# Optimization experiments

Measured on AMD Instinct MI355X. Metric: run time of the kernel, lower is better.

Reference implementation:

```python
import jax, jax.numpy as jnp
import numpy as np

DEPTH = 4
H1 = 64
H2 = 16
NF = 5
L = 10.0
K = 4
DIM = 3
N = 2048
NK = N // 4
FEAT = 1 + 2 * NF * DIM  # r scalar + Nf (cos,sin) pairs of dim components


def _tn(k, shape, std=0.01):
    return jax.random.truncated_normal(k, -2.0, 2.0, shape, jnp.float32) * std


def setup_inputs() -> dict:
    key = jax.random.key(0)
    ks = jax.random.split(key, 16)
    comb0 = 3 * DIM + 3 * FEAT   # combine width at depth 0
    combd = 3 * H1 + 3 * H2      # combine width at later depths
    return {
        "sx": jax.random.uniform(ks[0], (N, DIM), jnp.float32) * L,
        "kpoints": jax.random.normal(ks[1], (2 * NK, DIM), jnp.float32),
        "we0": _tn(ks[2], (comb0, H1)), "be0": jnp.zeros((H1,), jnp.float32),
        "we_rest": _tn(ks[3], (DEPTH - 1, combd, H1)), "be_rest": jnp.zeros((DEPTH - 1, H1), jnp.float32),
        "wee0": _tn(ks[4], (FEAT, H2)), "bee0": jnp.zeros((H2,), jnp.float32),
        "wee_rest": _tn(ks[5], (DEPTH - 2, H2, H2)), "bee_rest": jnp.zeros((DEPTH - 2, H2), jnp.float32),
        "wep0": _tn(ks[6], (FEAT, H2)), "bep0": jnp.zeros((H2,), jnp.float32),
        "wep_rest": _tn(ks[7], (DEPTH - 2, H2, H2)), "bep_rest": jnp.zeros((DEPTH - 2, H2), jnp.float32),
        "orb_w_re": _tn(ks[8], (H1, H1)), "orb_w_im": _tn(ks[9], (H1, H1)),
        "orb_b_re": jnp.zeros((H1,), jnp.float32), "orb_b_im": jnp.zeros((H1,), jnp.float32),
        "w_det": _tn(ks[10], (K, H1, H1)),
        "bf_w": _tn(ks[11], (H1, DIM)),
        "mlp_w1": _tn(ks[12], (DIM, H1)), "mlp_b1": jnp.zeros((H1,), jnp.float32),
        "mlp_w2": _tn(ks[13], (H1, K * (NK - 1))), "mlp_b2": jnp.zeros((K * (NK - 1),), jnp.float32),
    }


def _fourier(rij, r):
    # interleaved [r, cos1, sin1, ..., cosNf, sinNf] like the original
    feats = [r[..., None]]
    for k in range(1, NF + 1):
        ang = (2.0 * np.pi * k / L) * rij
        feats.append(jnp.cos(ang))
        feats.append(jnp.sin(ang))
    return jnp.concatenate(feats, axis=-1)


def _combine(e, ee, ep):
    mm = e.shape[0]
    h = mm // 2
    g1a = jnp.broadcast_to(jnp.mean(e[:h], 0, keepdims=True), e.shape)
    g1b = jnp.broadcast_to(jnp.mean(e[h:], 0, keepdims=True), e.shape)
    g2a = jnp.mean(ee[:h], axis=0)
    g2b = jnp.mean(ee[h:], axis=0)
    g3 = jnp.mean(ep, axis=1)
    return jnp.concatenate([e, g1a, g1b, g2a, g2b, g3], axis=1)


def _forward(sx, kpoints, we0, be0, we_rest, be_rest, wee0, bee0, wee_rest, bee_rest,
             wep0, bep0, wep_rest, bep_rest, orb_w_re, orb_w_im, orb_b_re, orb_b_im,
             w_det, bf_w, mlp_w1, mlp_b1, mlp_w2, mlp_b2):
    n, dim = sx.shape
    m, m2 = n // 2, n // 4
    s, x = sx[:m], sx[m:]
    e = jnp.broadcast_to(kpoints[0][None, :], (m, dim))
    # electron-electron pairwise features (m,m,FEAT)
    rij = x[:, None, :] - x[None, :, :]
    eye = jnp.eye(m, dtype=x.dtype)
    r = jnp.linalg.norm(jnp.sin(np.pi * rij / L) + eye[..., None], axis=-1) * (1.0 - eye) * (L / np.pi)
    ee = _fourier(rij, r)
    # electron-proton pairwise features (m,m,FEAT)
    rij = x[:, None, :] - s[None, :, :]
    r = jnp.linalg.norm(jnp.sin(np.pi * rij / L), axis=-1) * (L / np.pi)
    ep = _fourier(rij, r)
    for d in range(DEPTH - 1):
        f = _combine(e, ee, ep)
        We, be = (we0, be0) if d == 0 else (we_rest[d - 1], be_rest[d - 1])
        Wee, bee = (wee0, bee0) if d == 0 else (wee_rest[d - 1], bee_rest[d - 1])
        Wep, bep = (wep0, bep0) if d == 0 else (wep_rest[d - 1], bep_rest[d - 1])
        e_u = jnp.tanh(f @ We + be)
        ee_u = jnp.tanh(ee @ Wee + bee)
        ep_u = jnp.tanh(ep @ Wep + bep)
        e, ee, ep = (e_u + e, ee_u + ee, ep_u + ep) if d > 0 else (e_u, ee_u, ep_u)
    f = _combine(e, ee, ep)
    e = jnp.tanh(f @ we_rest[-1] + be_rest[-1]) + e
    # complex orbitals and geminal pairing matrix phi: (K, m2, m2)
    orb = e.astype(jnp.complex64) @ (orb_w_re + 1j * orb_w_im) + (orb_b_re + 1j * orb_b_im)
    phi = jnp.einsum('ia,kab,jb->kij', orb[:m2], w_det.astype(jnp.complex64), orb[m2:]) + 1.0
    # backflow coordinates and plane-wave determinant factors
    z = e @ bf_w + x
    nk = kpoints.shape[0] // 2
    norm = 1.0 / L ** (dim / 2)
    D_up = norm * jnp.exp(1j * jnp.einsum('kd,id->ki', kpoints[:nk], z[:m2]))  # (nk, m2)
    D_dn = norm * jnp.exp(1j * jnp.einsum('kd,id->ki', kpoints[nk:], z[m2:]))  # (nk, m2)
    h = jnp.tanh(kpoints[0] @ mlp_w1 + mlp_b1)
    fdet = jax.nn.softplus(h @ mlp_w2 + mlp_b2).reshape(K, nk - 1)
    fdet = jnp.concatenate([jnp.ones((K, 1), fdet.dtype), fdet], axis=1)  # (K, nk)
    D = jnp.einsum('ai,ka,aj->kij', D_up, fdet.astype(D_up.dtype), jnp.conj(D_dn))
    # logdet_matmul: stable log of signed sum of K determinants
    phase, logabs = jnp.linalg.slogdet(D * phi)
    maxl = jnp.max(logabs)
    det = jnp.sum(phase * jnp.exp(logabs - maxl))
    return jnp.log(jnp.abs(det)) + maxl + jnp.log(det / jnp.abs(det))


def reference(sx, kpoints, we0, be0, we_rest, be_rest, wee0, bee0, wee_rest, bee_rest,
              wep0, bep0, wep_rest, bep_rest, orb_w_re, orb_w_im, orb_b_re, orb_b_im,
              w_det, bf_w, mlp_w1, mlp_b1, mlp_w2, mlp_b2):
    return _forward(sx, kpoints, we0, be0, we_rest, be_rest, wee0, bee0, wee_rest, bee_rest,
                    wep0, bep0, wep_rest, bep_rest, orb_w_re, orb_w_im, orb_b_re, orb_b_im,
                    w_det, bf_w, mlp_w1, mlp_b1, mlp_w2, mlp_b2)
```

## Files before the change

### kernel.cpp

```cpp
#include <hip/hip_runtime.h>

typedef unsigned int uint;
typedef unsigned short ushort;

#define M1 1024
#define MH 512
#define PI_F 3.14159265358979323846f
#define LBOX 10.0f
#define NB 32

__device__ __forceinline__ float bf2f(ushort h){ return __uint_as_float(((uint)h)<<16); }
__device__ __forceinline__ ushort f2bf(float f){ uint u = __float_as_uint(f); uint r = (u + 0x7fffu + ((u>>16)&1u))>>16; return (ushort)r; }
__device__ __forceinline__ float ftanh(float x){ float e = __expf(2.f*x); return 1.f - 2.f/(e+1.f); }
__device__ __forceinline__ float2 cmul(float2 a, float2 b){ return make_float2(a.x*b.x - a.y*b.y, a.x*b.y + a.y*b.x); }
__device__ __forceinline__ void cfma(float2& c, float2 a, float2 b){
  c.x = fmaf(a.x,b.x,fmaf(-a.y,b.y,c.x));
  c.y = fmaf(a.x,b.y,fmaf(a.y,b.x,c.y));
}

__device__ __forceinline__ void fourier31(float d0, float d1, float d2, bool diag, float f[31]){
  const float k1 = PI_F / LBOX;
  float s[3], c[3];
  __sincosf(k1*d0, &s[0], &c[0]);
  __sincosf(k1*d1, &s[1], &c[1]);
  __sincosf(k1*d2, &s[2], &c[2]);
  float r = diag ? 0.f : (LBOX/PI_F)*sqrtf(s[0]*s[0]+s[1]*s[1]+s[2]*s[2]);
  f[0] = r;
  float cb[3], sb[3], cc[3], sc[3];
  #pragma unroll
  for (int d=0; d<3; ++d){ cb[d] = 1.f - 2.f*s[d]*s[d]; sb[d] = 2.f*s[d]*c[d]; cc[d]=cb[d]; sc[d]=sb[d]; }
  #pragma unroll
  for (int k=0;k<5;++k){
    #pragma unroll
    for (int d=0; d<3; ++d){ f[1+6*k+d] = cc[d]; f[4+6*k+d] = sc[d]; }
    if (k<4){
      #pragma unroll
      for (int d=0; d<3; ++d){
        float nc = cc[d]*cb[d]-sc[d]*sb[d];
        float ns = sc[d]*cb[d]+cc[d]*sb[d];
        cc[d]=nc; sc[d]=ns;
      }
    }
// ... 32 lines not shown
    ushort lo = f2bf(ftanh(acc[2*h]));
    ushort hi = f2bf(ftanh(acc[2*h+1]));
    u[h] = (uint)lo | ((uint)hi<<16);
  }
  uint4* dst = (uint4*)(out + ((size_t)i*M1 + j)*16);
  dst[0] = make_uint4(u[0],u[1],u[2],u[3]);
  dst[1] = make_uint4(u[4],u[5],u[6],u[7]);
  __shared__ float buf[256*33];
  #pragma unroll
  for (int c=0;c<31;++c) buf[threadIdx.x*33+c] = f[c];
  __syncthreads();
  #pragma unroll
  for (int s=128; s>0; s>>=1){
    if (threadIdx.x < s){
      #pragma unroll
      for (int c=0;c<31;++c) buf[threadIdx.x*33+c] += buf[(threadIdx.x+s)*33+c];
    }
    __syncthreads();
  }
  if (threadIdx.x < 31){
    float* g = (chunk >= 2) ? g2b : g2a;
    atomicAdd(&g[i*31+threadIdx.x], buf[threadIdx.x]);
  }
}

__global__ __launch_bounds__(256) void k_pair0ep(const float* __restrict__ sx,
    const float* __restrict__ W0, const float* __restrict__ b0,
    const float* __restrict__ W1, const float* __restrict__ b1,
    const float* __restrict__ W2, const float* __restrict__ b2,
    float* __restrict__ g3, float* __restrict__ gep1, float* __restrict__ gep2,
    float* __restrict__ gep3){
  int bx = blockIdx.x;
  int i = bx >> 2;
  int chunk = bx & 3;
  int j = (chunk << 8) + threadIdx.x;
  const float* xs = sx + 3*M1;
  float xi0 = xs[3*i], xi1 = xs[3*i+1], xi2 = xs[3*i+2];
  float y0 = sx[3*j], y1 = sx[3*j+1], y2 = sx[3*j+2];
  float f[31];
  fourier31(xi0-y0, xi1-y1, xi2-y2, false, f);
  float acc[16];
  #pragma unroll
  for (int o=0;o<16;++o) acc[o] = b0[o];
  #pragma unroll
  for (int c=0;c<31;++c){ float fv = f[c];
    #pragma unroll
    for (int o=0;o<16;++o) acc[o] = fmaf(fv, W0[c*16+o], acc[o]);
  }
  float hv[16];
  #pragma unroll
  for (int o=0;o<16;++o) hv[o] = ftanh(acc[o]);
  __shared__ float buf[256*49];
  #pragma unroll
  for (int c=0;c<31;++c) buf[threadIdx.x*49+c] = f[c];
  #pragma unroll
  for (int c=0;c<16;++c) buf[threadIdx.x*49+31+c] = hv[c];
  __syncthreads();
  #pragma unroll
  for (int s=128; s>0; s>>=1){
    if (threadIdx.x < s){
      #pragma unroll
      for (int c=0;c<47;++c) buf[threadIdx.x*49+c] += buf[(threadIdx.x+s)*49+c];
    }
    __syncthreads();
  }
  if (threadIdx.x < 31) atomicAdd(&g3[i*31+threadIdx.x], buf[threadIdx.x]);
  else if (threadIdx.x < 47) atomicAdd(&gep1[i*16 + (threadIdx.x-31)], buf[threadIdx.x]);
  float v1[16];
// ... 246 lines not shown
    __syncthreads();
    #pragma unroll
    for (int aa=0; aa<16; ++aa){
      float2 A0 = As[aa*32+i0], A1 = As[aa*32+i0+1];
      float2 B0 = Bs[aa*32+j0], B1 = Bs[aa*32+j0+16];
      cfma(a00,A0,B0); cfma(a01,A0,B1); cfma(a10,A1,B0); cfma(a11,A1,B1);
    }
    __syncthreads();
  }
  float2* Ts = sm;
  float2* Od = sm + 2080;
  for (int t = threadIdx.x; t < 2048; t += 256){
    int il = t >> 6, bc = t & 63;
    Ts[il*65+bc] = T[((size_t)k*512 + ib + il)*64 + bc];
    int oidx = (512 + jb + il)*64 + bc;
    Od[il*65+bc] = make_float2(ore[oidx], oim[oidx]);
  }
  __syncthreads();
  float2 p00={1,0},p01={1,0},p10={1,0},p11={1,0};
  #pragma unroll 8
  for (int bb=0; bb<64; ++bb){
    float2 T0 = Ts[i0*65+bb], T1 = Ts[(i0+1)*65+bb];
    float2 O0 = Od[j0*65+bb], O1 = Od[(j0+16)*65+bb];
    cfma(p00,T0,O0); cfma(p01,T0,O1); cfma(p10,T1,O0); cfma(p11,T1,O1);
  }
  size_t base = ((size_t)k*512 + ib + i0)*512 + jb;
  Mb[base+j0]        = cmul(a00, p00);
  Mb[base+j0+16]     = cmul(a01, p01);
  Mb[base+512+j0]    = cmul(a10, p10);
  Mb[base+512+j0+16] = cmul(a11, p11);
}

__global__ __launch_bounds__(512)
void k_panel(float2* __restrict__ Mb, float2* __restrict__ LinvG,
             int* __restrict__ rowmap, int* __restrict__ swapc, int col0){
  int k = blockIdx.x;
  float2* Mk = Mb + (size_t)k*512*512;
  int R = 512 - col0;
  int R64 = R < 64 ? R : 64;
  int rl = threadIdx.x;
  bool active = rl < R;
  int wv = rl >> 6;
  __shared__ float2 mir[64*33];
  __shared__ float2 Us[NB*33];
  __shared__ float2 dinv[NB];
  __shared__ float2 Ls[NB*NB];
  __shared__ float2 Yv[NB*NB];
  __shared__ int winslot[NB];
  __shared__ int newposS[64];
  int rm_orig = active ? rowmap[k*512 + col0 + rl] : 0;
  float2 X[NB];
  if (rl >= 64 && active){
    const float4* rp = (const float4*)(Mk + (size_t)rm_orig*512 + col0);
    #pragma unroll
    for (int q=0;q<NB/2;++q){ float4 v = rp[q]; X[2*q]=make_float2(v.x,v.y); X[2*q+1]=make_float2(v.z,v.w); }
  }
  if (wv == 0){
    if (rl < R64){
      const float4* rp = (const float4*)(Mk + (size_t)rm_orig*512 + col0);
      #pragma unroll
      for (int q=0;q<NB/2;++q){
        float4 v = rp[q];
        mir[rl*33+2*q]   = make_float2(v.x,v.y);
        mir[rl*33+2*q+1] = make_float2(v.z,v.w);
      }
    }
    bool done = false;
    int winpos = 0;
    for (int cc=0; cc<NB; ++cc){
      bool cand = (rl < R64) && !done;
      float2 cv = make_float2(0.f,0.f);
      if (cand) cv = mir[rl*33+cc];
      float val = cand ? fmaf(cv.x,cv.x,cv.y*cv.y) : -1.f;
      int idx = rl;
      #pragma unroll
      for (int off=32; off>0; off>>=1){
        float ov = __shfl_xor(val, off);
        int   oi = __shfl_xor(idx, off);
        if (ov > val || (ov == val && oi < idx)){ val = ov; idx = oi; }
      }
      int p = idx;
      if (rl == 0) winslot[cc] = p;
      if (rl == p){ done = true; winpos = cc; }
      float2 dg = mir[p*33+cc];
      float dn = 1.f/fmaf(dg.x,dg.x,dg.y*dg.y);
      float2 inv = make_float2(dg.x*dn, -dg.y*dn);
      if (cand && rl != p){
        float2 l = cmul(cv, inv);
        mir[rl*33+cc] = l;
        for (int j=cc+1; j<NB; ++j){
          float2 pr = mir[p*33+j];
          float2 xv = mir[rl*33+j];
          xv.x = fmaf(-l.x, pr.x, fmaf( l.y, pr.y, xv.x));
          xv.y = fmaf(-l.x, pr.y, fmaf(-l.y, pr.x, xv.y));
          mir[rl*33+j] = xv;
        }
      }
    }
    unsigned long long nwmask = __ballot(rl < R64 && !done);
    int np = 0;
    if (rl < R64){
      np = done ? winpos : (NB + (int)__popcll(nwmask & ((1ull<<rl)-1ull)));
      newposS[rl] = np;
      rowmap[k*512 + col0 + np] = rm_orig;
      float4* wp = (float4*)(Mk + (size_t)rm_orig*512 + col0);
      #pragma unroll
      for (int q=0;q<NB/2;++q){
        float2 a = mir[rl*33+2*q], bq = mir[rl*33+2*q+1];
        wp[q] = make_float4(a.x,a.y,bq.x,bq.y);
      }
    }
    {
      int cnt = 0;
      for (int t=0;t<R64;++t){
        int nt = newposS[t];
        if (rl < R64 && t > rl && nt < np) cnt++;
      }
      #pragma unroll
      for (int off=32; off>0; off>>=1) cnt += __shfl_xor(cnt, off);
      if (rl == 0) swapc[k] += cnt;
    }
    if (rl < NB){
      int ws = winslot[rl];
      #pragma unroll
      for (int j=0;j<NB;++j){
        float2 v = mir[ws*33+j];
        Us[rl*33+j] = v;
        float2 lv;
        if      (j <  rl) lv = v;
        else if (j == rl) lv = make_float2(1.f,0.f);
        else              lv = make_float2(0.f,0.f);
        Ls[rl*NB+j] = lv;
      }
      float2 d = Us[rl*33+rl];
      float dn = 1.f/fmaf(d.x,d.x,d.y*d.y);
      dinv[rl] = make_float2(d.x*dn, -d.y*dn);
    }
  }
  __syncthreads();
  if (rl >= 64 && active){
    #pragma unroll
    for (int j=0;j<NB;++j){
      float2 t = X[j];
      #pragma unroll
      for (int q=0;q<NB;++q){
        if (q < j){
          float2 u = Us[q*33+j];
          t.x = fmaf(-X[q].x, u.x, fmaf( X[q].y, u.y, t.x));
          t.y = fmaf(-X[q].x, u.y, fmaf(-X[q].y, u.x, t.y));
        }
      }
      X[j] = cmul(t, dinv[j]);
    }
    float4* wp = (float4*)(Mk + (size_t)rm_orig*512 + col0);
    #pragma unroll
    for (int q=0;q<NB/2;++q) wp[q] = make_float4(X[2*q].x,X[2*q].y,X[2*q+1].x,X[2*q+1].y);
  }
  if (rl < NB){
    for (int i=0;i<NB;++i){
      float2 acc = (i==rl)? make_float2(1.f,0.f) : make_float2(0.f,0.f);
      for (int q=rl; q<i; ++q){
        float2 lv = Ls[i*NB+q];
        float2 yv = Yv[q*NB+rl];
        acc.x = fmaf(-lv.x, yv.x, fmaf( lv.y, yv.y, acc.x));
        acc.y = fmaf(-lv.x, yv.y, fmaf(-lv.y, yv.x, acc.y));
      }
      Yv[i*NB+rl] = acc;
    }
  }
  __syncthreads();
  {
    float4* dst = (float4*)(LinvG + (size_t)k*(NB*NB));
    const float4* src = (const float4*)Yv;
    for (int q=rl; q<NB*NB/2; q+=blockDim.x) dst[q] = src[q];
  }
}

__global__ __launch_bounds__(256) void k_gemm(float2* __restrict__ Mb, const float2* __restrict__ LinvG,
                                              const int* __restrict__ rowmap, int col0){
  int k = blockIdx.z;
  float2* Mk = Mb + (size_t)k*512*512;
  int e0 = col0 + NB;
  int r0 = e0 + blockIdx.x*32;
  int j0c = e0 + blockIdx.y*32;
  int tid = threadIdx.x;
  int jl = tid & 31, rg = tid >> 5;
  __shared__ float2 As[NB*33];
  __shared__ float2 Bs[NB*33];
  __shared__ float2 Av[NB*33];
  __shared__ float2 Li[NB*NB];
  __shared__ int prA[32];
  __shared__ int prB[NB];
  if (tid < 32) prA[tid] = rowmap[k*512 + r0 + tid];
  else if (tid < 64) prB[tid-32] = rowmap[k*512 + col0 + (tid-32)];
  {
    const float4* src = (const float4*)(LinvG + (size_t)k*(NB*NB));
    float4* dst = (float4*)Li;
    for (int q=tid; q<NB*NB/2; q+=256) dst[q] = src[q];
  }
  __syncthreads();
  #pragma unroll
  for (int s=0;s<4;++s){
    int a = rg + 8*s;
    Av[a*33 + jl] = Mk[(size_t)prB[a]*512 + j0c + jl];
  }
  for (int t=tid; t<1024; t+=256){
    int rl = t >> 5, kk = t & 31;
    As[kk*33+rl] = Mk[(size_t)prA[rl]*512 + col0 + kk];
  }
  __syncthreads();
  #pragma unroll
  for (int s=0;s<4;++s){
    int m = rg + 8*s;
    float2 acc = make_float2(0.f,0.f);
    #pragma unroll 8
    for (int a=0;a<NB;++a) cfma(acc, Li[m*NB+a], Av[a*33+jl]);
    Bs[m*33+jl] = acc;
  }
  __syncthreads();
  int i0 = (tid >> 4)*2, j0 = (tid & 15)*2;
  float2 a00={0,0},a01={0,0},a10={0,0},a11={0,0};
  #pragma unroll 16
  for (int kk=0;kk<NB;++kk){
    float2 A0 = As[kk*33+i0], A1 = As[kk*33+i0+1];
    float2 B0 = Bs[kk*33+j0], B1 = Bs[kk*33+j0+1];
    cfma(a00,A0,B0); cfma(a01,A0,B1); cfma(a10,A1,B0); cfma(a11,A1,B1);
  }
  size_t ro0 = (size_t)prA[i0]*512 + j0c + j0;
  size_t ro1 = (size_t)prA[i0+1]*512 + j0c + j0;
  float2 c0 = Mk[ro0];   c0.x-=a00.x; c0.y-=a00.y; Mk[ro0]=c0;
  float2 c1 = Mk[ro0+1]; c1.x-=a01.x; c1.y-=a01.y; Mk[ro0+1]=c1;
  float2 c2 = Mk[ro1];   c2.x-=a10.x; c2.y-=a10.y; Mk[ro1]=c2;
  float2 c3 = Mk[ro1+1]; c3.x-=a11.x; c3.y-=a11.y; Mk[ro1+1]=c3;
}

__global__ void k_det(const float2* __restrict__ Mb, const int* __restrict__ rowmap,
                      const int* __restrict__ swapc, float* __restrict__ out, int out_size){
  int tid = threadIdx.x;
  int k = tid >> 6, lane = tid & 63;
  const float2* Mk = Mb + (size_t)k*512*512;
  double la = 0.0, ang = 0.0;
  for (int q=0;q<8;++q){
    int i = lane*8 + q;
    int pr = rowmap[k*512 + i];
    float2 u = Mk[(size_t)pr*512+i];
    double re = (double)u.x, im = (double)u.y;
    la += 0.5*log(re*re + im*im);
    ang += atan2(im, re);
  }
  #pragma unroll
  for (int off=32; off>0; off>>=1){
    la += __shfl_down(la, off);
    ang += __shfl_down(ang, off);
  }
  __shared__ double las[4], angs[4];
  if (lane==0){
    las[k] = la;
    angs[k] = ang + 3.14159265358979323846*(double)(swapc[k] & 1);
  }
  __syncthreads();
  if (tid==0){
    double mx = las[0];
    for (int q=1;q<4;++q) mx = fmax(mx, las[q]);
    double sre=0.0, sim=0.0;
    for (int q=0;q<4;++q){
      double w = exp(las[q]-mx);
      sre += w*cos(angs[q]);
      sim += w*sin(angs[q]);
    }
    double mag = sqrt(sre*sre+sim*sim);
    out[0] = (float)(log(mag)+mx);
    if (out_size > 1) out[1] = (float)atan2(sim, sre);
    for (int q=2;q<out_size;++q) out[q] = 0.f;
  }
}

extern "C" void kernel_launch(void* const* d_in, const int* in_sizes, int n_in,
                              void* d_out, int out_size, void* d_ws, size_t ws_size,
                              hipStream_t stream){
  const float* sx   = (const float*)d_in[0];
  const float* kp   = (const float*)d_in[1];
  const float* we0  = (const float*)d_in[2];
  const float* be0  = (const float*)d_in[3];
  const float* weR  = (const float*)d_in[4];
  const float* beR  = (const float*)d_in[5];
  const float* wee0 = (const float*)d_in[6];
  const float* bee0 = (const float*)d_in[7];
  const float* weeR = (const float*)d_in[8];
  const float* beeR = (const float*)d_in[9];
  const float* wep0 = (const float*)d_in[10];
  const float* bep0 = (const float*)d_in[11];
  const float* wepR = (const float*)d_in[12];
  const float* bepR = (const float*)d_in[13];
  const float* owre = (const float*)d_in[14];
  const float* owim = (const float*)d_in[15];
  const float* obre = (const float*)d_in[16];
  const float* obim = (const float*)d_in[17];
  const float* wdet = (const float*)d_in[18];
  const float* bfw  = (const float*)d_in[19];
  const float* mw1  = (const float*)d_in[20];
  const float* mb1  = (const float*)d_in[21];
  const float* mw2  = (const float*)d_in[22];
  const float* mb2  = (const float*)d_in[23];

  char* ws = (char*)d_ws;
  size_t off = 0;
  auto alloc = [&](size_t bytes)->char*{
    char* p = ws + off;
    off = (off + bytes + 255) & ~(size_t)255;
    return p;
  };
  ushort* ee   = (ushort*)alloc(33554432);
  float2* Mb   = (float2*)alloc(8388608);
  float2* U    = (float2*)alloc(2097152);
  float2* V    = (float2*)alloc(2097152);
  float2* T    = (float2*)alloc(1048576);
  float*  eS   = (float*)alloc(1048576);
  float*  ore  = (float*)alloc(262144);
  float*  oim  = (float*)alloc(262144);
  float*  z    = (float*)alloc(12288);
  float*  fdet = (float*)alloc(8192);
  float2* Linv = (float2*)alloc(131072);
  int*    rowmap = (int*)alloc(8192);
  char*   zst  = ws + off;
  float*  g2a0 = (float*)alloc(126976);
  float*  g2b0 = (float*)alloc(126976);
  float*  g30  = (float*)alloc(126976);
  float*  geeA = (float*)alloc(196608);
  float*  geeB = (float*)alloc(196608);
  float*  gep  = (float*)alloc(196608);
  float*  g1s  = (float*)alloc(1536);
  int*    swpc = (int*)alloc(16);
  int zn = (int)(((char*)(swpc+4) - zst)/4);

  float* e1 = eS;           float* e2 = eS + 65536;
  float* e3 = eS + 131072;  float* e4 = eS + 196608;
  float* geeA1 = geeA;      float* geeA2 = geeA+16384; float* geeA3 = geeA+32768;
  float* geeB1 = geeB;      float* geeB2 = geeB+16384; float* geeB3 = geeB+32768;
  float* gep1  = gep;       float* gep2  = gep+16384;  float* gep3  = gep+32768;
  float* g1s1 = g1s; float* g1s2 = g1s+128; float* g1s3 = g1s+256;

  k_init<<<256,256,0,stream>>>((float*)zst, zn, rowmap);
  k_pair0ee<<<4096,256,0,stream>>>(sx, wee0, bee0, ee, g2a0, g2b0);
  k_pair0ep<<<4096,256,0,stream>>>(sx, wep0, bep0, wepR, bepR, wepR+256, bepR+16,
                                   g30, gep1, gep2, gep3);
  k_e0<<<256,256,0,stream>>>(kp, g2a0, g2b0, g30, we0, be0, e1, g1s1);
  k_gee<<<128,256,0,stream>>>(ee, geeA1, geeB1);
  k_eupd<<<256,256,0,stream>>>(e1, e2, weR, beR, g1s1, geeA1, geeB1, gep1, g1s2);
  k_pairU<<<4096,256,0,stream>>>(ee, weeR, beeR);
  k_gee<<<128,256,0,stream>>>(ee, geeA2, geeB2);
  k_eupd<<<256,256,0,stream>>>(e2, e3, weR+240*64, beR+64, g1s2, geeA2, geeB2, gep2, g1s3);
  k_pairU<<<4096,256,0,stream>>>(ee, weeR+256, beeR+16);
  k_gee<<<128,256,0,stream>>>(ee, geeA3, geeB3);
  k_eupd<<<256,256,0,stream>>>(e3, e4, weR+2*240*64, beR+128, g1s3, geeA3, geeB3, gep3, nullptr);
  k_orbz<<<256,256,0,stream>>>(e4, owre, owim, obre, obim, bfw, sx, ore, oim, z);
  k_uvTf<<<2568,256,0,stream>>>(kp, z, ore, oim, wdet, mw1, mb1, mw2, mb2, U, V, T, fdet);
  k_M<<<1024,256,0,stream>>>(U, V, fdet, T, ore, oim, Mb);
  for (int tpan=0;tpan<16;++tpan){
    int col0 = tpan*NB;
    int R = 512 - col0;
    int Rpad = (R + 63) & ~63;
    k_panel<<<4, Rpad, 0, stream>>>(Mb, Linv, rowmap, swpc, col0);
    if (tpan < 15){
      int nch = 15 - tpan;
      k_gemm<<<dim3(nch,nch,4),256,0,stream>>>(Mb, Linv, rowmap, col0);
    }
  }
  k_det<<<1,256,0,stream>>>(Mb, rowmap, swpc, (float*)d_out, out_size);
  (void)in_sizes; (void)n_in; (void)ws_size;
}
```

Baseline: 1.844 ms.

## Fuse blocked LU panel, trailing update and det into one persistent kernel

Replaces the 31 alternating panel/GEMM launches and the final determinant launch with a single persistent kernel of 256 blocks. The blocks step through the panels and separate the phases with an atomic-counter grid barrier. Trailing-update tiles are distributed across blocks in a strided job loop. This removes per-launch overhead on the sequential LU chain, but it relies on all 256 blocks being co-resident and adds spin-barrier cost. Panel steps also use only 4 of the 256 blocks while the rest wait.

```diff
diff --git a/kernel.cpp b/kernel.cpp
--- a/kernel.cpp
+++ b/kernel.cpp
@@ -420,246 +420,273 @@
 }
 
 __global__ __launch_bounds__(512)
-void k_panel(float2* __restrict__ Mb, float2* __restrict__ LinvG,
-             int* __restrict__ rowmap, int* __restrict__ swapc, int col0){
-  int k = blockIdx.x;
-  float2* Mk = Mb + (size_t)k*512*512;
-  int R = 512 - col0;
-  int R64 = R < 64 ? R : 64;
-  int rl = threadIdx.x;
-  bool active = rl < R;
-  int wv = rl >> 6;
-  __shared__ float2 mir[64*33];
-  __shared__ float2 Us[NB*33];
+void k_lu(float2* __restrict__ Mb, float2* __restrict__ LinvG,
+          int* __restrict__ rowmap, int* __restrict__ swapc,
+          int* __restrict__ bar, float* __restrict__ out, int out_size){
+  int bid = blockIdx.x;
+  int tid = threadIdx.x;
+  __shared__ float2 smA[64*33];
+  __shared__ float2 smB[32*33];
+  __shared__ float2 smC[32*32];
+  __shared__ float2 smD[32*32];
   __shared__ float2 dinv[NB];
-  __shared__ float2 Ls[NB*NB];
-  __shared__ float2 Yv[NB*NB];
   __shared__ int winslot[NB];
   __shared__ int newposS[64];
-  int rm_orig = active ? rowmap[k*512 + col0 + rl] : 0;
-  float2 X[NB];
-  if (rl >= 64 && active){
-    const float4* rp = (const float4*)(Mk + (size_t)rm_orig*512 + col0);
-    #pragma unroll
-    for (int q=0;q<NB/2;++q){ float4 v = rp[q]; X[2*q]=make_float2(v.x,v.y); X[2*q+1]=make_float2(v.z,v.w); }
-  }
-  if (wv == 0){
-    if (rl < R64){
-      const float4* rp = (const float4*)(Mk + (size_t)rm_orig*512 + col0);
-      #pragma unroll
-      for (int q=0;q<NB/2;++q){
-        float4 v = rp[q];
-        mir[rl*33+2*q]   = make_float2(v.x,v.y);
-        mir[rl*33+2*q+1] = make_float2(v.z,v.w);
-      }
-    }
-    bool done = false;
-    int winpos = 0;
-    for (int cc=0; cc<NB; ++cc){
-      bool cand = (rl < R64) && !done;
-      float2 cv = make_float2(0.f,0.f);
-      if (cand) cv = mir[rl*33+cc];
-      float val = cand ? fmaf(cv.x,cv.x,cv.y*cv.y) : -1.f;
-      int idx = rl;
+  __shared__ int prA[32];
+  __shared__ int prB[32];
+  __shared__ double las[4], angs[4];
+  int ph = 0;
+  const int G = (int)gridDim.x;
+
+  for (int t=0; t<16; ++t){
+    int col0 = t*NB;
+    if (bid < 4){
+      int k = bid;
+      float2* Mk = Mb + (size_t)k*512*512;
+      int R = 512 - col0;
+      int R64 = R < 64 ? R : 64;
+      int rl = tid;
+      bool active = rl < R;
+      int wv = rl >> 6;
+      float2* mir = smA;
+      float2* Us  = smB;
+      float2* Ls  = smC;
+      float2* Yv  = smD;
+      int rm_orig = active ? rowmap[k*512 + col0 + rl] : 0;
+      float2 X[NB];
+      if (rl >= 64 && active){
+        const float4* rp = (const float4*)(Mk + (size_t)rm_orig*512 + col0);
+        #pragma unroll
+        for (int q=0;q<NB/2;++q){ float4 v = rp[q]; X[2*q]=make_float2(v.x,v.y); X[2*q+1]=make_float2(v.z,v.w); }
+      }
+      if (wv == 0){
+        if (rl < R64){
+          const float4* rp = (const float4*)(Mk + (size_t)rm_orig*512 + col0);
+          #pragma unroll
+          for (int q=0;q<NB/2;++q){
+            float4 v = rp[q];
+            mir[rl*33+2*q]   = make_float2(v.x,v.y);
+            mir[rl*33+2*q+1] = make_float2(v.z,v.w);
+          }
+        }
+        bool done = false;
+        int winpos = 0;
+        for (int cc=0; cc<NB; ++cc){
+          bool cand = (rl < R64) && !done;
+          float2 cv = make_float2(0.f,0.f);
+          if (cand) cv = mir[rl*33+cc];
+          float val = cand ? fmaf(cv.x,cv.x,cv.y*cv.y) : -1.f;
+          int idx = rl;
+          #pragma unroll
+          for (int off=32; off>0; off>>=1){
+            float ov = __shfl_xor(val, off);
+            int   oi = __shfl_xor(idx, off);
+            if (ov > val || (ov == val && oi < idx)){ val = ov; idx = oi; }
+          }
+          int p = idx;
+          if (rl == 0) winslot[cc] = p;
+          if (rl == p){ done = true; winpos = cc; }
+          float2 dg = mir[p*33+cc];
+          float dn = 1.f/fmaf(dg.x,dg.x,dg.y*dg.y);
+          float2 inv = make_float2(dg.x*dn, -dg.y*dn);
+          if (cand && rl != p){
+            float2 l = cmul(cv, inv);
+            mir[rl*33+cc] = l;
+            for (int j=cc+1; j<NB; ++j){
+              float2 pr = mir[p*33+j];
+              float2 xv = mir[rl*33+j];
+              xv.x = fmaf(-l.x, pr.x, fmaf( l.y, pr.y, xv.x));
+              xv.y = fmaf(-l.x, pr.y, fmaf(-l.y, pr.x, xv.y));
+              mir[rl*33+j] = xv;
+            }
+          }
+        }
+        unsigned long long nwmask = __ballot(rl < R64 && !done);
+        int np = 0;
+        if (rl < R64){
+          np = done ? winpos : (NB + (int)__popcll(nwmask & ((1ull<<rl)-1ull)));
+          newposS[rl] = np;
+          rowmap[k*512 + col0 + np] = rm_orig;
+          float4* wp = (float4*)(Mk + (size_t)rm_orig*512 + col0);
+          #pragma unroll
+          for (int q=0;q<NB/2;++q){
+            float2 a = mir[rl*33+2*q], bq = mir[rl*33+2*q+1];
+            wp[q] = make_float4(a.x,a.y,bq.x,bq.y);
+          }
+        }
+        {
+          int cnt = 0;
+          for (int tt=0;tt<R64;++tt){
+            int nt = newposS[tt];
+            if (rl < R64 && tt > rl && nt < np) cnt++;
+          }
+          #pragma unroll
+          for (int off=32; off>0; off>>=1) cnt += __shfl_xor(cnt, off);
+          if (rl == 0) swapc[k] += cnt;
+        }
+        if (rl < NB){
+          int ws = winslot[rl];
+          #pragma unroll
+          for (int j=0;j<NB;++j){
+            float2 v = mir[ws*33+j];
+            Us[rl*33+j] = v;
+            float2 lv;
+            if      (j <  rl) lv = v;
+            else if (j == rl) lv = make_float2(1.f,0.f);
+            else              lv = make_float2(0.f,0.f);
+            Ls[rl*NB+j] = lv;
+          }
+          float2 d = Us[rl*33+rl];
+          float dn = 1.f/fmaf(d.x,d.x,d.y*d.y);
+          dinv[rl] = make_float2(d.x*dn, -d.y*dn);
+        }
+      }
+      __syncthreads();
+      if (rl >= 64 && active){
+        #pragma unroll
+        for (int j=0;j<NB;++j){
+          float2 tt = X[j];
+          #pragma unroll
+          for (int q=0;q<NB;++q){
+            if (q < j){
+              float2 u = Us[q*33+j];
+              tt.x = fmaf(-X[q].x, u.x, fmaf( X[q].y, u.y, tt.x));
+              tt.y = fmaf(-X[q].x, u.y, fmaf(-X[q].y, u.x, tt.y));
+            }
+          }
+          X[j] = cmul(tt, dinv[j]);
+        }
+        float4* wp = (float4*)(Mk + (size_t)rm_orig*512 + col0);
+        #pragma unroll
+        for (int q=0;q<NB/2;++q) wp[q] = make_float4(X[2*q].x,X[2*q].y,X[2*q+1].x,X[2*q+1].y);
+      }
+      if (rl < NB){
+        for (int i=0;i<NB;++i){
+          float2 acc = (i==rl)? make_float2(1.f,0.f) : make_float2(0.f,0.f);
+          for (int q=rl; q<i; ++q){
+            float2 lv = Ls[i*NB+q];
+            float2 yv = Yv[q*NB+rl];
+            acc.x = fmaf(-lv.x, yv.x, fmaf( lv.y, yv.y, acc.x));
+            acc.y = fmaf(-lv.x, yv.y, fmaf(-lv.y, yv.x, acc.y));
+          }
+          Yv[i*NB+rl] = acc;
+        }
+      }
+      __syncthreads();
+      ((float4*)(LinvG + (size_t)k*(NB*NB)))[rl] = ((const float4*)Yv)[rl];
+    }
+    ph++;
+    __threadfence();
+    __syncthreads();
+    if (tid == 0){
+      atomicAdd(bar, 1);
+      while (__hip_atomic_load(bar, __ATOMIC_RELAXED, __HIP_MEMORY_SCOPE_AGENT) < ph*G)
+        __builtin_amdgcn_s_sleep(2);
+    }
+    __syncthreads();
+    __threadfence();
+    if (t < 15){
+      int nch = 15 - t;
+      int e0 = col0 + NB;
+      int jobs = 4*nch*nch;
+      float2* Av = smA;
+      float2* Bs = smA + 1056;
+      float2* As = smB;
+      float2* Li = smC;
+      int jl = tid & 31;
+      int rg = tid >> 5;
+      for (int job = bid; job < jobs; job += G){
+        int kq = job / (nch*nch);
+        int rem = job - kq*nch*nch;
+        int bx = rem / nch, by = rem - bx*nch;
+        float2* Mk = Mb + (size_t)kq*512*512;
+        int r0 = e0 + bx*32;
+        int j0c = e0 + by*32;
+        if (tid < 32) prA[tid] = rowmap[kq*512 + r0 + tid];
+        else if (tid < 64) prB[tid-32] = rowmap[kq*512 + col0 + (tid-32)];
+        ((float4*)Li)[tid] = ((const float4*)(LinvG + (size_t)kq*(NB*NB)))[tid];
+        __syncthreads();
+        Av[rg*33+jl]      = Mk[(size_t)prB[rg]*512 + j0c + jl];
+        Av[(rg+16)*33+jl] = Mk[(size_t)prB[rg+16]*512 + j0c + jl];
+        #pragma unroll
+        for (int s2=0;s2<2;++s2){
+          int t2 = tid + 512*s2;
+          int rl2 = t2 >> 5, kk2 = t2 & 31;
+          As[kk2*33 + rl2] = Mk[(size_t)prA[rl2]*512 + col0 + kk2];
+        }
+        __syncthreads();
+        #pragma unroll
+        for (int s2=0;s2<2;++s2){
+          int m = rg + 16*s2;
+          float2 acc = make_float2(0.f,0.f);
+          #pragma unroll 8
+          for (int a=0;a<NB;++a) cfma(acc, Li[m*NB+a], Av[a*33+jl]);
+          Bs[m*33+jl] = acc;
+        }
+        __syncthreads();
+        float2 acc0 = make_float2(0.f,0.f), acc1 = make_float2(0.f,0.f);
+        #pragma unroll 16
+        for (int kk=0;kk<NB;++kk){
+          float2 B0 = Bs[kk*33+jl];
+          cfma(acc0, As[kk*33+rg], B0);
+          cfma(acc1, As[kk*33+rg+16], B0);
+        }
+        size_t ro0 = (size_t)prA[rg]*512 + j0c + jl;
+        size_t ro1 = (size_t)prA[rg+16]*512 + j0c + jl;
+        float2 c0 = Mk[ro0]; c0.x-=acc0.x; c0.y-=acc0.y; Mk[ro0]=c0;
+        float2 c1 = Mk[ro1]; c1.x-=acc1.x; c1.y-=acc1.y; Mk[ro1]=c1;
+        __syncthreads();
+      }
+      ph++;
+      __threadfence();
+      __syncthreads();
+      if (tid == 0){
+        atomicAdd(bar, 1);
+        while (__hip_atomic_load(bar, __ATOMIC_RELAXED, __HIP_MEMORY_SCOPE_AGENT) < ph*G)
+          __builtin_amdgcn_s_sleep(2);
+      }
+      __syncthreads();
+      __threadfence();
+    }
+  }
+  if (bid == 0){
+    double la = 0.0, ang = 0.0;
+    if (tid < 256){
+      int kq = tid >> 6, lane = tid & 63;
+      const float2* Mk = Mb + (size_t)kq*512*512;
+      for (int q=0;q<8;++q){
+        int i = lane*8 + q;
+        int pr = rowmap[kq*512 + i];
+        float2 u = Mk[(size_t)pr*512+i];
+        double re = (double)u.x, im = (double)u.y;
+        la += 0.5*log(re*re + im*im);
+        ang += atan2(im, re);
+      }
       #pragma unroll
       for (int off=32; off>0; off>>=1){
-        float ov = __shfl_xor(val, off);
-        int   oi = __shfl_xor(idx, off);
-        if (ov > val || (ov == val && oi < idx)){ val = ov; idx = oi; }
-      }
-      int p = idx;
-      if (rl == 0) winslot[cc] = p;
-      if (rl == p){ done = true; winpos = cc; }
-      float2 dg = mir[p*33+cc];
-      float dn = 1.f/fmaf(dg.x,dg.x,dg.y*dg.y);
-      float2 inv = make_float2(dg.x*dn, -dg.y*dn);
-      if (cand && rl != p){
-        float2 l = cmul(cv, inv);
-        mir[rl*33+cc] = l;
-        for (int j=cc+1; j<NB; ++j){
-          float2 pr = mir[p*33+j];
-          float2 xv = mir[rl*33+j];
-          xv.x = fmaf(-l.x, pr.x, fmaf( l.y, pr.y, xv.x));
-          xv.y = fmaf(-l.x, pr.y, fmaf(-l.y, pr.x, xv.y));
-          mir[rl*33+j] = xv;
-        }
-      }
-    }
-    unsigned long long nwmask = __ballot(rl < R64 && !done);
-    int np = 0;
-    if (rl < R64){
-      np = done ? winpos : (NB + (int)__popcll(nwmask & ((1ull<<rl)-1ull)));
-      newposS[rl] = np;
-      rowmap[k*512 + col0 + np] = rm_orig;
-      float4* wp = (float4*)(Mk + (size_t)rm_orig*512 + col0);
-      #pragma unroll
-      for (int q=0;q<NB/2;++q){
-        float2 a = mir[rl*33+2*q], bq = mir[rl*33+2*q+1];
-        wp[q] = make_float4(a.x,a.y,bq.x,bq.y);
-      }
-    }
-    {
-      int cnt = 0;
-      for (int t=0;t<R64;++t){
-        int nt = newposS[t];
-        if (rl < R64 && t > rl && nt < np) cnt++;
-      }
-      #pragma unroll
-      for (int off=32; off>0; off>>=1) cnt += __shfl_xor(cnt, off);
-      if (rl == 0) swapc[k] += cnt;
-    }
-    if (rl < NB){
-      int ws = winslot[rl];
-      #pragma unroll
-      for (int j=0;j<NB;++j){
-        float2 v = mir[ws*33+j];
-        Us[rl*33+j] = v;
-        float2 lv;
-        if      (j <  rl) lv = v;
-        else if (j == rl) lv = make_float2(1.f,0.f);
-        else              lv = make_float2(0.f,0.f);
-        Ls[rl*NB+j] = lv;
-      }
-      float2 d = Us[rl*33+rl];
-      float dn = 1.f/fmaf(d.x,d.x,d.y*d.y);
-      dinv[rl] = make_float2(d.x*dn, -d.y*dn);
-    }
-  }
-  __syncthreads();
-  if (rl >= 64 && active){
-    #pragma unroll
-    for (int j=0;j<NB;++j){
-      float2 t = X[j];
-      #pragma unroll
-      for (int q=0;q<NB;++q){
-        if (q < j){
-          float2 u = Us[q*33+j];
-          t.x = fmaf(-X[q].x, u.x, fmaf( X[q].y, u.y, t.x));
-          t.y = fmaf(-X[q].x, u.y, fmaf(-X[q].y, u.x, t.y));
-        }
-      }
-      X[j] = cmul(t, dinv[j]);
-    }
-    float4* wp = (float4*)(Mk + (size_t)rm_orig*512 + col0);
-    #pragma unroll
-    for (int q=0;q<NB/2;++q) wp[q] = make_float4(X[2*q].x,X[2*q].y,X[2*q+1].x,X[2*q+1].y);
-  }
-  if (rl < NB){
-    for (int i=0;i<NB;++i){
-      float2 acc = (i==rl)? make_float2(1.f,0.f) : make_float2(0.f,0.f);
-      for (int q=rl; q<i; ++q){
-        float2 lv = Ls[i*NB+q];
-        float2 yv = Yv[q*NB+rl];
-        acc.x = fmaf(-lv.x, yv.x, fmaf( lv.y, yv.y, acc.x));
-        acc.y = fmaf(-lv.x, yv.y, fmaf(-lv.y, yv.x, acc.y));
-      }
-      Yv[i*NB+rl] = acc;
-    }
-  }
-  __syncthreads();
-  {
-    float4* dst = (float4*)(LinvG + (size_t)k*(NB*NB));
-    const float4* src = (const float4*)Yv;
-    for (int q=rl; q<NB*NB/2; q+=blockDim.x) dst[q] = src[q];
-  }
-}
-
-__global__ __launch_bounds__(256) void k_gemm(float2* __restrict__ Mb, const float2* __restrict__ LinvG,
-                                              const int* __restrict__ rowmap, int col0){
-  int k = blockIdx.z;
-  float2* Mk = Mb + (size_t)k*512*512;
-  int e0 = col0 + NB;
-  int r0 = e0 + blockIdx.x*32;
-  int j0c = e0 + blockIdx.y*32;
-  int tid = threadIdx.x;
-  int jl = tid & 31, rg = tid >> 5;
-  __shared__ float2 As[NB*33];
-  __shared__ float2 Bs[NB*33];
-  __shared__ float2 Av[NB*33];
-  __shared__ float2 Li[NB*NB];
-  __shared__ int prA[32];
-  __shared__ int prB[NB];
-  if (tid < 32) prA[tid] = rowmap[k*512 + r0 + tid];
-  else if (tid < 64) prB[tid-32] = rowmap[k*512 + col0 + (tid-32)];
-  {
-    const float4* src = (const float4*)(LinvG + (size_t)k*(NB*NB));
-    float4* dst = (float4*)Li;
-    for (int q=tid; q<NB*NB/2; q+=256) dst[q] = src[q];
-  }
-  __syncthreads();
-  #pragma unroll
-  for (int s=0;s<4;++s){
-    int a = rg + 8*s;
-    Av[a*33 + jl] = Mk[(size_t)prB[a]*512 + j0c + jl];
-  }
-  for (int t=tid; t<1024; t+=256){
-    int rl = t >> 5, kk = t & 31;
-    As[kk*33+rl] = Mk[(size_t)prA[rl]*512 + col0 + kk];
-  }
-  __syncthreads();
-  #pragma unroll
-  for (int s=0;s<4;++s){
-    int m = rg + 8*s;
-    float2 acc = make_float2(0.f,0.f);
-    #pragma unroll 8
-    for (int a=0;a<NB;++a) cfma(acc, Li[m*NB+a], Av[a*33+jl]);
-    Bs[m*33+jl] = acc;
-  }
-  __syncthreads();
-  int i0 = (tid >> 4)*2, j0 = (tid & 15)*2;
-  float2 a00={0,0},a01={0,0},a10={0,0},a11={0,0};
-  #pragma unroll 16
-  for (int kk=0;kk<NB;++kk){
-    float2 A0 = As[kk*33+i0], A1 = As[kk*33+i0+1];
-    float2 B0 = Bs[kk*33+j0], B1 = Bs[kk*33+j0+1];
-    cfma(a00,A0,B0); cfma(a01,A0,B1); cfma(a10,A1,B0); cfma(a11,A1,B1);
-  }
-  size_t ro0 = (size_t)prA[i0]*512 + j0c + j0;
-  size_t ro1 = (size_t)prA[i0+1]*512 + j0c + j0;
-  float2 c0 = Mk[ro0];   c0.x-=a00.x; c0.y-=a00.y; Mk[ro0]=c0;
-  float2 c1 = Mk[ro0+1]; c1.x-=a01.x; c1.y-=a01.y; Mk[ro0+1]=c1;
-  float2 c2 = Mk[ro1];   c2.x-=a10.x; c2.y-=a10.y; Mk[ro1]=c2;
-  float2 c3 = Mk[ro1+1]; c3.x-=a11.x; c3.y-=a11.y; Mk[ro1+1]=c3;
-}
-
-__global__ void k_det(const float2* __restrict__ Mb, const int* __restrict__ rowmap,
-                      const int* __restrict__ swapc, float* __restrict__ out, int out_size){
-  int tid = threadIdx.x;
-  int k = tid >> 6, lane = tid & 63;
-  const float2* Mk = Mb + (size_t)k*512*512;
-  double la = 0.0, ang = 0.0;
-  for (int q=0;q<8;++q){
-    int i = lane*8 + q;
-    int pr = rowmap[k*512 + i];
-    float2 u = Mk[(size_t)pr*512+i];
-    double re = (double)u.x, im = (double)u.y;
-    la += 0.5*log(re*re + im*im);
-    ang += atan2(im, re);
-  }
-  #pragma unroll
-  for (int off=32; off>0; off>>=1){
-    la += __shfl_down(la, off);
-    ang += __shfl_down(ang, off);
-  }
-  __shared__ double las[4], angs[4];
-  if (lane==0){
-    las[k] = la;
-    angs[k] = ang + 3.14159265358979323846*(double)(swapc[k] & 1);
-  }
-  __syncthreads();
-  if (tid==0){
-    double mx = las[0];
-    for (int q=1;q<4;++q) mx = fmax(mx, las[q]);
-    double sre=0.0, sim=0.0;
-    for (int q=0;q<4;++q){
-      double w = exp(las[q]-mx);
-      sre += w*cos(angs[q]);
-      sim += w*sin(angs[q]);
-    }
-    double mag = sqrt(sre*sre+sim*sim);
-    out[0] = (float)(log(mag)+mx);
-    if (out_size > 1) out[1] = (float)atan2(sim, sre);
-    for (int q=2;q<out_size;++q) out[q] = 0.f;
+        la += __shfl_down(la, off);
+        ang += __shfl_down(ang, off);
+      }
+      if (lane==0){
+        las[kq] = la;
+        angs[kq] = ang + 3.14159265358979323846*(double)(swapc[kq] & 1);
+      }
+    }
+    __syncthreads();
+    if (tid==0){
+      double mx = las[0];
+      for (int q=1;q<4;++q) mx = fmax(mx, las[q]);
+      double sre=0.0, sim=0.0;
+      for (int q=0;q<4;++q){
+        double w = exp(las[q]-mx);
+        sre += w*cos(angs[q]);
+        sim += w*sin(angs[q]);
+      }
+      double mag = sqrt(sre*sre+sim*sim);
+      out[0] = (float)(log(mag)+mx);
+      if (out_size > 1) out[1] = (float)atan2(sim, sre);
+      for (int q=2;q<out_size;++q) out[q] = 0.f;
+    }
   }
 }
 
@@ -719,7 +746,8 @@
   float*  gep  = (float*)alloc(196608);
   float*  g1s  = (float*)alloc(1536);
   int*    swpc = (int*)alloc(16);
-  int zn = (int)(((char*)(swpc+4) - zst)/4);
+  int*    bar  = (int*)alloc(256);
+  int zn = (int)(((char*)bar + 256 - zst)/4);
 
   float* e1 = eS;           float* e2 = eS + 65536;
   float* e3 = eS + 131072;  float* e4 = eS + 196608;
@@ -744,16 +772,6 @@
   k_orbz<<<256,256,0,stream>>>(e4, owre, owim, obre, obim, bfw, sx, ore, oim, z);
   k_uvTf<<<2568,256,0,stream>>>(kp, z, ore, oim, wdet, mw1, mb1, mw2, mb2, U, V, T, fdet);
   k_M<<<1024,256,0,stream>>>(U, V, fdet, T, ore, oim, Mb);
-  for (int tpan=0;tpan<16;++tpan){
-    int col0 = tpan*NB;
-    int R = 512 - col0;
-    int Rpad = (R + 63) & ~63;
-    k_panel<<<4, Rpad, 0, stream>>>(Mb, Linv, rowmap, swpc, col0);
-    if (tpan < 15){
-      int nch = 15 - tpan;
-      k_gemm<<<dim3(nch,nch,4),256,0,stream>>>(Mb, Linv, rowmap, col0);
-    }
-  }
-  k_det<<<1,256,0,stream>>>(Mb, rowmap, swpc, (float*)d_out, out_size);
+  k_lu<<<256,512,0,stream>>>(Mb, Linv, rowmap, swpc, bar, (float*)d_out, out_size);
   (void)in_sizes; (void)n_in; (void)ws_size;
 }
```

New measurement: 3.683 ms. 99.8% more time.

## Widen LU panel block from 32 to 64 columns, halving panel/GEMM launches

Applied to the files above, without the earlier changes.

Raises the blocked-LU panel width to 64, so each panel factors 64 rows by pivot search with the whole wave and does the trailing triangular solve in two 32-column halves. Only 8 panel and 7 GEMM rounds are launched instead of 16 and 15, which cuts the serial launch and sync chain of the complex LU factorization. The cost is a longer serial pivot loop per panel, more shared memory and registers in the panel kernel, and a deeper inner dimension in the GEMM. The separate L buffer is dropped and read straight from the mirror array.

```diff
diff --git a/kernel.cpp b/kernel.cpp
--- a/kernel.cpp
+++ b/kernel.cpp
@@ -7,7 +7,7 @@
 #define MH 512
 #define PI_F 3.14159265358979323846f
 #define LBOX 10.0f
-#define NB 32
+#define NB 64
 
 __device__ __forceinline__ float bf2f(ushort h){ return __uint_as_float(((uint)h)<<16); }
 __device__ __forceinline__ ushort f2bf(float f){ uint u = __float_as_uint(f); uint r = (u + 0x7fffu + ((u>>16)&1u))>>16; return (ushort)r; }
@@ -106,8 +106,7 @@
     float* __restrict__ gep3){
   int bx = blockIdx.x;
   int i = bx >> 2;
-  int chunk = bx & 3;
-  int j = (chunk << 8) + threadIdx.x;
+  int j = ((bx & 3) << 8) + threadIdx.x;
   const float* xs = sx + 3*M1;
   float xi0 = xs[3*i], xi1 = xs[3*i+1], xi2 = xs[3*i+2];
   float y0 = sx[3*j], y1 = sx[3*j+1], y2 = sx[3*j+2];
@@ -424,41 +423,29 @@
              int* __restrict__ rowmap, int* __restrict__ swapc, int col0){
   int k = blockIdx.x;
   float2* Mk = Mb + (size_t)k*512*512;
-  int R = 512 - col0;
-  int R64 = R < 64 ? R : 64;
   int rl = threadIdx.x;
-  bool active = rl < R;
   int wv = rl >> 6;
-  __shared__ float2 mir[64*33];
-  __shared__ float2 Us[NB*33];
-  __shared__ float2 dinv[NB];
-  __shared__ float2 Ls[NB*NB];
-  __shared__ float2 Yv[NB*NB];
-  __shared__ int winslot[NB];
+  __shared__ float2 mir[64*65];
+  __shared__ float2 Us[64*65];
+  __shared__ float2 Yv[64*64];
+  __shared__ float2 dinv[64];
+  __shared__ int winslot[64];
   __shared__ int newposS[64];
-  int rm_orig = active ? rowmap[k*512 + col0 + rl] : 0;
-  float2 X[NB];
-  if (rl >= 64 && active){
+  int rm_orig = rowmap[k*512 + col0 + rl];
+  if (wv == 0){
     const float4* rp = (const float4*)(Mk + (size_t)rm_orig*512 + col0);
     #pragma unroll
-    for (int q=0;q<NB/2;++q){ float4 v = rp[q]; X[2*q]=make_float2(v.x,v.y); X[2*q+1]=make_float2(v.z,v.w); }
-  }
-  if (wv == 0){
-    if (rl < R64){
-      const float4* rp = (const float4*)(Mk + (size_t)rm_orig*512 + col0);
-      #pragma unroll
-      for (int q=0;q<NB/2;++q){
-        float4 v = rp[q];
-        mir[rl*33+2*q]   = make_float2(v.x,v.y);
-        mir[rl*33+2*q+1] = make_float2(v.z,v.w);
-      }
+    for (int q=0;q<32;++q){
+      float4 v = rp[q];
+      mir[rl*65+2*q]   = make_float2(v.x,v.y);
+      mir[rl*65+2*q+1] = make_float2(v.z,v.w);
     }
     bool done = false;
     int winpos = 0;
-    for (int cc=0; cc<NB; ++cc){
-      bool cand = (rl < R64) && !done;
+    for (int cc=0; cc<64; ++cc){
+      bool cand = !done;
       float2 cv = make_float2(0.f,0.f);
-      if (cand) cv = mir[rl*33+cc];
+      if (cand) cv = mir[rl*65+cc];
       float val = cand ? fmaf(cv.x,cv.x,cv.y*cv.y) : -1.f;
       int idx = rl;
       #pragma unroll
@@ -470,97 +457,123 @@
       int p = idx;
       if (rl == 0) winslot[cc] = p;
       if (rl == p){ done = true; winpos = cc; }
-      float2 dg = mir[p*33+cc];
+      float2 dg = mir[p*65+cc];
       float dn = 1.f/fmaf(dg.x,dg.x,dg.y*dg.y);
       float2 inv = make_float2(dg.x*dn, -dg.y*dn);
       if (cand && rl != p){
         float2 l = cmul(cv, inv);
-        mir[rl*33+cc] = l;
-        for (int j=cc+1; j<NB; ++j){
-          float2 pr = mir[p*33+j];
-          float2 xv = mir[rl*33+j];
+        mir[rl*65+cc] = l;
+        for (int j=cc+1; j<64; ++j){
+          float2 pr = mir[p*65+j];
+          float2 xv = mir[rl*65+j];
           xv.x = fmaf(-l.x, pr.x, fmaf( l.y, pr.y, xv.x));
           xv.y = fmaf(-l.x, pr.y, fmaf(-l.y, pr.x, xv.y));
-          mir[rl*33+j] = xv;
+          mir[rl*65+j] = xv;
         }
       }
     }
-    unsigned long long nwmask = __ballot(rl < R64 && !done);
-    int np = 0;
-    if (rl < R64){
-      np = done ? winpos : (NB + (int)__popcll(nwmask & ((1ull<<rl)-1ull)));
-      newposS[rl] = np;
-      rowmap[k*512 + col0 + np] = rm_orig;
-      float4* wp = (float4*)(Mk + (size_t)rm_orig*512 + col0);
-      #pragma unroll
-      for (int q=0;q<NB/2;++q){
-        float2 a = mir[rl*33+2*q], bq = mir[rl*33+2*q+1];
-        wp[q] = make_float4(a.x,a.y,bq.x,bq.y);
-      }
+    newposS[rl] = winpos;
+    rowmap[k*512 + col0 + winpos] = rm_orig;
+    float4* wp = (float4*)(Mk + (size_t)rm_orig*512 + col0);
+    #pragma unroll
+    for (int q=0;q<32;++q){
+      float2 a = mir[rl*65+2*q], bq = mir[rl*65+2*q+1];
+      wp[q] = make_float4(a.x,a.y,bq.x,bq.y);
     }
     {
       int cnt = 0;
-      for (int t=0;t<R64;++t){
-        int nt = newposS[t];
-        if (rl < R64 && t > rl && nt < np) cnt++;
-      }
+      for (int t2=rl+1; t2<64; ++t2) if (newposS[t2] < winpos) cnt++;
       #pragma unroll
       for (int off=32; off>0; off>>=1) cnt += __shfl_xor(cnt, off);
       if (rl == 0) swapc[k] += cnt;
     }
-    if (rl < NB){
+    {
       int ws = winslot[rl];
-      #pragma unroll
-      for (int j=0;j<NB;++j){
-        float2 v = mir[ws*33+j];
-        Us[rl*33+j] = v;
-        float2 lv;
-        if      (j <  rl) lv = v;
-        else if (j == rl) lv = make_float2(1.f,0.f);
-        else              lv = make_float2(0.f,0.f);
-        Ls[rl*NB+j] = lv;
-      }
-      float2 d = Us[rl*33+rl];
+      #pragma unroll 8
+      for (int j=0;j<64;++j) Us[rl*65+j] = mir[ws*65+j];
+      float2 d = Us[rl*65+rl];
       float dn = 1.f/fmaf(d.x,d.x,d.y*d.y);
       dinv[rl] = make_float2(d.x*dn, -d.y*dn);
     }
   }
   __syncthreads();
-  if (rl >= 64 && active){
-    #pragma unroll
-    for (int j=0;j<NB;++j){
+  if (rl >= 64){
+    float2 X[32];
+    {
+      const float4* rpA = (const float4*)(Mk + (size_t)rm_orig*512 + col0);
+      #pragma unroll
+      for (int q=0;q<16;++q){ float4 v = rpA[q]; X[2*q]=make_float2(v.x,v.y); X[2*q+1]=make_float2(v.z,v.w); }
+    }
+    #pragma unroll
+    for (int j=0;j<32;++j){
       float2 t = X[j];
       #pragma unroll
-      for (int q=0;q<NB;++q){
+      for (int q=0;q<32;++q){
         if (q < j){
-          float2 u = Us[q*33+j];
+          float2 u = Us[q*65+j];
           t.x = fmaf(-X[q].x, u.x, fmaf( X[q].y, u.y, t.x));
           t.y = fmaf(-X[q].x, u.y, fmaf(-X[q].y, u.x, t.y));
         }
       }
       X[j] = cmul(t, dinv[j]);
     }
-    float4* wp = (float4*)(Mk + (size_t)rm_orig*512 + col0);
-    #pragma unroll
-    for (int q=0;q<NB/2;++q) wp[q] = make_float4(X[2*q].x,X[2*q].y,X[2*q+1].x,X[2*q+1].y);
-  }
-  if (rl < NB){
-    for (int i=0;i<NB;++i){
+    {
+      float4* wpA = (float4*)(Mk + (size_t)rm_orig*512 + col0);
+      #pragma unroll
+      for (int q=0;q<16;++q) wpA[q] = make_float4(X[2*q].x,X[2*q].y,X[2*q+1].x,X[2*q+1].y);
+    }
+    float2 X2[32];
+    {
+      const float4* rpB = (const float4*)(Mk + (size_t)rm_orig*512 + col0 + 32);
+      #pragma unroll
+      for (int q=0;q<16;++q){ float4 v = rpB[q]; X2[2*q]=make_float2(v.x,v.y); X2[2*q+1]=make_float2(v.z,v.w); }
+    }
+    for (int q=0;q<32;++q){
+      float2 x1 = Mk[(size_t)rm_orig*512 + col0 + q];
+      #pragma unroll
+      for (int j=0;j<32;++j){
+        float2 u = Us[q*65+32+j];
+        X2[j].x = fmaf(-x1.x, u.x, fmaf( x1.y, u.y, X2[j].x));
+        X2[j].y = fmaf(-x1.x, u.y, fmaf(-x1.y, u.x, X2[j].y));
+      }
+    }
+    #pragma unroll
+    for (int j=0;j<32;++j){
+      float2 t = X2[j];
+      #pragma unroll
+      for (int q=0;q<32;++q){
+        if (q < j){
+          float2 u = Us[(32+q)*65+32+j];
+          t.x = fmaf(-X2[q].x, u.x, fmaf( X2[q].y, u.y, t.x));
+          t.y = fmaf(-X2[q].x, u.y, fmaf(-X2[q].y, u.x, t.y));
+        }
+      }
+      X2[j] = cmul(t, dinv[32+j]);
+    }
+    {
+      float4* wpB = (float4*)(Mk + (size_t)rm_orig*512 + col0 + 32);
+      #pragma unroll
+      for (int q=0;q<16;++q) wpB[q] = make_float4(X2[2*q].x,X2[2*q].y,X2[2*q+1].x,X2[2*q+1].y);
+    }
+  }
+  if (rl < 64){
+    for (int i=0;i<64;++i){
       float2 acc = (i==rl)? make_float2(1.f,0.f) : make_float2(0.f,0.f);
+      int wsi = winslot[i];
       for (int q=rl; q<i; ++q){
-        float2 lv = Ls[i*NB+q];
-        float2 yv = Yv[q*NB+rl];
+        float2 lv = mir[wsi*65+q];
+        float2 yv = Yv[q*64+rl];
         acc.x = fmaf(-lv.x, yv.x, fmaf( lv.y, yv.y, acc.x));
         acc.y = fmaf(-lv.x, yv.y, fmaf(-lv.y, yv.x, acc.y));
       }
-      Yv[i*NB+rl] = acc;
+      Yv[i*64+rl] = acc;
     }
   }
   __syncthreads();
   {
-    float4* dst = (float4*)(LinvG + (size_t)k*(NB*NB));
+    float4* dst = (float4*)(LinvG + (size_t)k*4096);
     const float4* src = (const float4*)Yv;
-    for (int q=rl; q<NB*NB/2; q+=blockDim.x) dst[q] = src[q];
+    for (int q=rl; q<2048; q+=blockDim.x) dst[q] = src[q];
   }
 }
 
@@ -573,53 +586,53 @@
   int j0c = e0 + blockIdx.y*32;
   int tid = threadIdx.x;
   int jl = tid & 31, rg = tid >> 5;
-  __shared__ float2 As[NB*33];
-  __shared__ float2 Bs[NB*33];
-  __shared__ float2 Av[NB*33];
-  __shared__ float2 Li[NB*NB];
+  __shared__ float2 As[64*33];
+  __shared__ float2 Bs[64*33];
+  __shared__ float2 Av[64*33];
+  __shared__ float2 Li[64*64];
   __shared__ int prA[32];
-  __shared__ int prB[NB];
+  __shared__ int prB[64];
   if (tid < 32) prA[tid] = rowmap[k*512 + r0 + tid];
-  else if (tid < 64) prB[tid-32] = rowmap[k*512 + col0 + (tid-32)];
+  else if (tid < 96) prB[tid-32] = rowmap[k*512 + col0 + (tid-32)];
   {
-    const float4* src = (const float4*)(LinvG + (size_t)k*(NB*NB));
+    const float4* src = (const float4*)(LinvG + (size_t)k*4096);
     float4* dst = (float4*)Li;
-    for (int q=tid; q<NB*NB/2; q+=256) dst[q] = src[q];
-  }
-  __syncthreads();
-  #pragma unroll
-  for (int s=0;s<4;++s){
+    for (int q=tid; q<2048; q+=256) dst[q] = src[q];
+  }
+  __syncthreads();
+  #pragma unroll
+  for (int s=0;s<8;++s){
     int a = rg + 8*s;
     Av[a*33 + jl] = Mk[(size_t)prB[a]*512 + j0c + jl];
   }
-  for (int t=tid; t<1024; t+=256){
-    int rl = t >> 5, kk = t & 31;
-    As[kk*33+rl] = Mk[(size_t)prA[rl]*512 + col0 + kk];
-  }
-  __syncthreads();
-  #pragma unroll
-  for (int s=0;s<4;++s){
+  for (int t=tid; t<2048; t+=256){
+    int rl2 = t >> 6, kk2 = t & 63;
+    As[kk2*33 + rl2] = Mk[(size_t)prA[rl2]*512 + col0 + kk2];
+  }
+  __syncthreads();
+  #pragma unroll
+  for (int s=0;s<8;++s){
     int m = rg + 8*s;
     float2 acc = make_float2(0.f,0.f);
-    #pragma unroll 8
-    for (int a=0;a<NB;++a) cfma(acc, Li[m*NB+a], Av[a*33+jl]);
+    #pragma unroll 16
+    for (int a=0;a<64;++a) cfma(acc, Li[m*64+a], Av[a*33+jl]);
     Bs[m*33+jl] = acc;
   }
   __syncthreads();
-  int i0 = (tid >> 4)*2, j0 = (tid & 15)*2;
+  int i0 = (tid >> 4)*2, j0 = tid & 15;
   float2 a00={0,0},a01={0,0},a10={0,0},a11={0,0};
   #pragma unroll 16
-  for (int kk=0;kk<NB;++kk){
+  for (int kk=0;kk<64;++kk){
     float2 A0 = As[kk*33+i0], A1 = As[kk*33+i0+1];
-    float2 B0 = Bs[kk*33+j0], B1 = Bs[kk*33+j0+1];
+    float2 B0 = Bs[kk*33+j0], B1 = Bs[kk*33+j0+16];
     cfma(a00,A0,B0); cfma(a01,A0,B1); cfma(a10,A1,B0); cfma(a11,A1,B1);
   }
-  size_t ro0 = (size_t)prA[i0]*512 + j0c + j0;
-  size_t ro1 = (size_t)prA[i0+1]*512 + j0c + j0;
-  float2 c0 = Mk[ro0];   c0.x-=a00.x; c0.y-=a00.y; Mk[ro0]=c0;
-  float2 c1 = Mk[ro0+1]; c1.x-=a01.x; c1.y-=a01.y; Mk[ro0+1]=c1;
-  float2 c2 = Mk[ro1];   c2.x-=a10.x; c2.y-=a10.y; Mk[ro1]=c2;
-  float2 c3 = Mk[ro1+1]; c3.x-=a11.x; c3.y-=a11.y; Mk[ro1+1]=c3;
+  size_t ro0 = (size_t)prA[i0]*512 + j0c;
+  size_t ro1 = (size_t)prA[i0+1]*512 + j0c;
+  float2 c0 = Mk[ro0+j0];    c0.x-=a00.x; c0.y-=a00.y; Mk[ro0+j0]=c0;
+  float2 c1 = Mk[ro0+j0+16]; c1.x-=a01.x; c1.y-=a01.y; Mk[ro0+j0+16]=c1;
+  float2 c2 = Mk[ro1+j0];    c2.x-=a10.x; c2.y-=a10.y; Mk[ro1+j0]=c2;
+  float2 c3 = Mk[ro1+j0+16]; c3.x-=a11.x; c3.y-=a11.y; Mk[ro1+j0+16]=c3;
 }
 
 __global__ void k_det(const float2* __restrict__ Mb, const int* __restrict__ rowmap,
@@ -744,14 +757,13 @@
   k_orbz<<<256,256,0,stream>>>(e4, owre, owim, obre, obim, bfw, sx, ore, oim, z);
   k_uvTf<<<2568,256,0,stream>>>(kp, z, ore, oim, wdet, mw1, mb1, mw2, mb2, U, V, T, fdet);
   k_M<<<1024,256,0,stream>>>(U, V, fdet, T, ore, oim, Mb);
-  for (int tpan=0;tpan<16;++tpan){
+  for (int tpan=0;tpan<8;++tpan){
     int col0 = tpan*NB;
     int R = 512 - col0;
-    int Rpad = (R + 63) & ~63;
-    k_panel<<<4, Rpad, 0, stream>>>(Mb, Linv, rowmap, swpc, col0);
-    if (tpan < 15){
-      int nch = 15 - tpan;
-      k_gemm<<<dim3(nch,nch,4),256,0,stream>>>(Mb, Linv, rowmap, col0);
+    k_panel<<<4, R, 0, stream>>>(Mb, Linv, rowmap, swpc, col0);
+    if (tpan < 7){
+      int n32 = 2*(7 - tpan);
+      k_gemm<<<dim3(n32,n32,4),256,0,stream>>>(Mb, Linv, rowmap, col0);
     }
   }
   k_det<<<1,256,0,stream>>>(Mb, rowmap, swpc, (float*)d_out, out_size);
```

Measured after the change: 2.493 ms. +35.2%, slower.
